# Kernel optimization log

Hardware: AMD Instinct MI355X
Metric: run time of the kernel (lower is better)

The kernel has to match this reference:

```python
import jax, jax.numpy as jnp
import numpy as np

B, P, D, H, A, C = 256, 512, 16, 256, 8, 2
HID = 256
IN_MLP = H + A + 1  # 265


def setup_inputs() -> dict:
    key = jax.random.key(0)
    ks = jax.random.split(key, 12)
    s = 0.05  # small init for recurrent stability
    return {
        "particles": jax.random.normal(ks[0], (B, P, D), jnp.float32),
        "weights": jax.random.uniform(ks[1], (B, P), jnp.float32),
        "actions": jax.random.normal(ks[2], (B, A), jnp.float32),
        "time": jax.random.uniform(ks[3], (B,), jnp.float32) * 100.0,
        "Wi": jax.random.normal(ks[4], (D + 1, 3 * H), jnp.float32) * s,
        "bi": jnp.zeros((3 * H,), jnp.float32),
        "Wh_rz": jax.random.normal(ks[5], (H, 2 * H), jnp.float32) * s,
        "Wh_n": jax.random.normal(ks[6], (H, H), jnp.float32) * s,
        "bn": jnp.zeros((H,), jnp.float32),
        "mlp_W1": jax.random.normal(ks[7], (C, IN_MLP, HID), jnp.float32) * s,
        "mlp_b1": jnp.zeros((C, HID), jnp.float32),
        "mlp_W2": jax.random.normal(ks[8], (C, HID, HID), jnp.float32) * s,
        "mlp_b2": jnp.zeros((C, HID), jnp.float32),
        "mlp_W3": jax.random.normal(ks[9], (C, HID, 1), jnp.float32) * s,
        "mlp_b3": jnp.zeros((C, 1), jnp.float32),
        "num_time_steps": 100,
    }


def reference(particles, weights, actions, time, Wi, bi, Wh_rz, Wh_n, bn,
              mlp_W1, mlp_b1, mlp_W2, mlp_b2, mlp_W3, mlp_b3, num_time_steps):
    # feature_fn = identity; append weights as an extra feature channel
    x = jnp.concatenate([particles, weights[..., None]], axis=-1)  # [B, P, D+1]
    xs = jnp.swapaxes(x, 0, 1)  # [P, B, D+1], scan over particle axis

    def gru_step(h, xt):
        gi = xt @ Wi + bi  # [B, 3H]
        i_r, i_z, i_n = jnp.split(gi, 3, axis=-1)
        hrz = h @ Wh_rz  # [B, 2H], no bias (flax GRUCell hidden r/z dense)
        r = jax.nn.sigmoid(i_r + hrz[:, :H])
        z = jax.nn.sigmoid(i_z + hrz[:, H:])
        n = jnp.tanh(i_n + r * (h @ Wh_n + bn))
        h_new = (1.0 - z) * n + z * h
        return h_new, None

    h0 = jnp.zeros((particles.shape[0], H), particles.dtype)
    enc, _ = jax.lax.scan(gru_step, h0, xs)  # last hidden == take(outputs, -1, axis=-2)

    norm_time = time / num_time_steps
    hidden = jnp.concatenate([enc, actions, norm_time[..., None]], axis=-1)  # [B, IN_MLP]

    # n_critics MLPs evaluated batched over critic axis c
    h1 = jax.nn.relu(jnp.einsum('bi,cio->bco', hidden, mlp_W1) + mlp_b1)
    h2 = jax.nn.relu(jnp.einsum('bci,cio->bco', h1, mlp_W2) + mlp_b2)
    q = jnp.einsum('bci,cio->bco', h2, mlp_W3) + mlp_b3  # [B, C, 1]
    return q[..., 0]  # [B, C]
```

## Files before the change

### kernel.cpp

```cpp
#include <hip/hip_runtime.h>
#include <hip/hip_fp16.h>

typedef _Float16 h2v __attribute__((ext_vector_type(2)));
typedef _Float16 f16x8 __attribute__((ext_vector_type(8)));
typedef float f32x4 __attribute__((ext_vector_type(4)));
typedef unsigned int u32;
typedef unsigned short u16;

#define NB 256
#define NP 512
#define NH 256

#define OFF_WH 0
#define LEN_WH 98304
#define OFF_WIB (OFF_WH + LEN_WH)
#define LEN_WIB 12288
#define OFF_W1 (OFF_WIB + LEN_WIB)
#define LEN_W1 68096
#define OFF_W2 (OFF_W1 + LEN_W1)
#define LEN_W2 65536
#define OFF_W3 (OFF_W2 + LEN_W2)
#define LEN_W3 256
#define WS_DWORDS (OFF_W3 + LEN_W3)

__device__ __forceinline__ u32 pack2(float lo, float hi) {
    h2v v; v.x = (_Float16)lo; v.y = (_Float16)hi;
    return __builtin_bit_cast(u32, v);
}

__device__ __forceinline__ float fdot2(u32 a, u32 b, float c) {
#if __has_builtin(__builtin_amdgcn_fdot2)
    return __builtin_amdgcn_fdot2(__builtin_bit_cast(h2v, a),
                                  __builtin_bit_cast(h2v, b), c, false);
#else
    h2v x = __builtin_bit_cast(h2v, a), y = __builtin_bit_cast(h2v, b);
    return c + (float)x.x * (float)y.x + (float)x.y * (float)y.y;
#endif
}

__global__ __launch_bounds__(256) void pack_kernel(
    const float* __restrict__ Wi, const float* __restrict__ Whrz,
    const float* __restrict__ Whn, const float* __restrict__ W1,
    const float* __restrict__ W2, const float* __restrict__ W3,
    u32* __restrict__ ws)
{
    for (int F = blockIdx.x * 256 + threadIdx.x; F < WS_DWORDS; F += gridDim.x * 256) {
        u32 val;
        if (F < OFF_WIB) {
            int l = F & 63; int t = F >> 6;
            int i = t % 192; int w = t / 192;
            int g = i >> 6; int tt = i & 63;
            int col = g * 256 + w * 32 + (l & 31);
            int k = ((l >> 5) << 7) + 2 * tt;
            float lo, hi;
            if (col < 512) { lo = Whrz[k * 512 + col]; hi = Whrz[(k + 1) * 512 + col]; }
            else { lo = Whn[k * 256 + (col - 512)]; hi = Whn[(k + 1) * 256 + (col - 512)]; }
            val = pack2(lo, hi);
        } else if (F < OFF_W1) {
            int j = F - OFF_WIB;
            int d = j & 3; int r = j >> 2;
            int l = r & 63; int q = r >> 6;
            int t = q % 6; int w = q / 6;
            int g = t >> 1, c = t & 1;
            int k = ((l >> 4) << 3) + 2 * d;
            int col = g * 256 + w * 32 + c * 16 + (l & 15);
            float lo = (k < 17) ? Wi[k * 768 + col] : 0.f;
            float hi = (k + 1 < 17) ? Wi[(k + 1) * 768 + col] : 0.f;
            val = pack2(lo, hi);
        } else if (F < OFF_W2) {
            int j = F - OFF_W1; int c = j / (133 * 256); int r = j % (133 * 256);
            int kk = r >> 8; int o = r & 255;
            int k = 2 * kk;
            float lo = W1[(c * 265 + k) * 256 + o];
            float hi = (k + 1 < 265) ? W1[(c * 265 + k + 1) * 256 + o] : 0.f;
            val = pack2(lo, hi);
        } else if (F < OFF_W3) {
            int j = F - OFF_W2; int c = j >> 15; int r = j & 32767;
            int kk = r >> 8; int o = r & 255;
            float lo = W2[(c * 256 + 2 * kk) * 256 + o];
            float hi = W2[(c * 256 + 2 * kk + 1) * 256 + o];
            val = pack2(lo, hi);
        } else {
            int j = F - OFF_W3; int c = j >> 7; int jj = j & 127;
            float lo = W3[c * 256 + 2 * jj];
            float hi = W3[c * 256 + 2 * jj + 1];
            val = pack2(lo, hi);
        }
        ws[F] = val;
    }
}

__global__ __launch_bounds__(512, 2) void qnet_kernel(
    const float* __restrict__ particles, const float* __restrict__ pweights,
    const float* __restrict__ actions, const float* __restrict__ timev,
    const float* __restrict__ bi, const float* __restrict__ bn,
    const float* __restrict__ b1, const float* __restrict__ b2,
    const float* __restrict__ b3, const int* __restrict__ nts,
    const u32* __restrict__ ws, float* __restrict__ out)
{
    __shared__ __align__(16) u32 sX[NP * 16];
    __shared__ __align__(16) float sG[8 * 1536];
    __shared__ __align__(16) u16 sH2[2][NH];
    __shared__ __align__(16) float sHf[NH];
    __shared__ __align__(16) float sMisc[16];

    const int b = blockIdx.x;
    const int tid = threadIdx.x;
    const int lane = tid & 63;
    const int wid = tid >> 6;

    u32 wreg[192];
    {
        const u32* gp = ws + OFF_WH + (wid * 192) * 64 + lane;
        #pragma unroll
        for (int i = 0; i < 192; ++i) wreg[i] = gp[i * 64];
    }
    {
        const float2* pr2 = (const float2*)(particles + (long)b * NP * 16);
        for (int j = tid; j < NP * 8; j += 512) {
            int p = j >> 3, q = j & 7;
            float2 v = pr2[j];
            sX[p * 16 + q] = pack2(v.x, v.y);
        }
        const float* wr = pweights + (long)b * NP;
        for (int j = tid; j < NP * 8; j += 512) {
            int p = j >> 3, q = j & 7;
            sX[p * 16 + 8 + q] = (q == 0) ? pack2(wr[p], 0.f) : 0u;
        }
    }
    if (tid < 256) ((u32*)sH2)[tid] = 0u;
    if (tid < 8) sMisc[tid] = actions[b * 8 + tid];
    if (tid == 8) sMisc[8] = timev[b] / (float)nts[0];

    float birL = 0.f, bizL = 0.f, binnL = 0.f, bnnL = 0.f, hreg = 0.f;
    if (lane < 32) {
        int j = wid * 32 + lane;
        birL = bi[j]; bizL = bi[NH + j]; binnL = bi[2 * NH + j]; bnnL = bn[j];
    }
    __syncthreads();

    const uint4* wibp = (const uint4*)(ws + OFF_WIB) + (wid * 6) * 64 + lane;

    #pragma unroll 1
    for (int p = 0; p < NP; ++p) {
        if ((p & 15) == 0) {
            f16x8 av = __builtin_bit_cast(f16x8,
                ((const uint4*)sX)[(p + (lane & 15)) * 4 + (lane >> 4)]);
            f32x4 z4 = {0.f, 0.f, 0.f, 0.f};
            int sb = (lane >> 4) << 2;
            float* gw = sG + wid * 1536 + (lane & 15);
            {
                f32x4 g0 = __builtin_amdgcn_mfma_f32_16x16x32_f16(av, __builtin_bit_cast(f16x8, wibp[0 * 64]), z4, 0, 0, 0);
                f32x4 g1 = __builtin_amdgcn_mfma_f32_16x16x32_f16(av, __builtin_bit_cast(f16x8, wibp[1 * 64]), z4, 0, 0, 0);
                #pragma unroll
                for (int r = 0; r < 4; ++r) {
                    gw[(sb + r) * 32]      = g0[r];
                    gw[(sb + r) * 32 + 16] = g1[r];
                }
            }
            {
                f32x4 g2 = __builtin_amdgcn_mfma_f32_16x16x32_f16(av, __builtin_bit_cast(f16x8, wibp[2 * 64]), z4, 0, 0, 0);
                f32x4 g3 = __builtin_amdgcn_mfma_f32_16x16x32_f16(av, __builtin_bit_cast(f16x8, wibp[3 * 64]), z4, 0, 0, 0);
                #pragma unroll
                for (int r = 0; r < 4; ++r) {
                    gw[512 + (sb + r) * 32]      = g2[r];
                    gw[512 + (sb + r) * 32 + 16] = g3[r];
                }
            }
            {
                f32x4 g4 = __builtin_amdgcn_mfma_f32_16x16x32_f16(av, __builtin_bit_cast(f16x8, wibp[4 * 64]), z4, 0, 0, 0);
                f32x4 g5 = __builtin_amdgcn_mfma_f32_16x16x32_f16(av, __builtin_bit_cast(f16x8, wibp[5 * 64]), z4, 0, 0, 0);
                #pragma unroll
                for (int r = 0; r < 4; ++r) {
                    gw[1024 + (sb + r) * 32]      = g4[r];
                    gw[1024 + (sb + r) * 32 + 16] = g5[r];
                }
            }
            __syncthreads();
        }

        float gR, gZ, gN;
        {
            const float* gp = sG + wid * 1536 + (p & 15) * 32 + (lane & 31);
            gR = gp[0]; gZ = gp[512]; gN = gp[1024];
        }

        const u32* hsrc = (const u32*)(&sH2[p & 1][0]) + ((lane >> 5) << 6);
        float aR = 0.f, aZ = 0.f, aN = 0.f;
        #pragma unroll
        for (int c = 0; c < 8; ++c) {
            uint4 h0 = ((const uint4*)hsrc)[2 * c];
            uint4 h1 = ((const uint4*)hsrc)[2 * c + 1];
            u32 hv[8] = {h0.x, h0.y, h0.z, h0.w, h1.x, h1.y, h1.z, h1.w};
            #pragma unroll
            for (int j = 0; j < 8; ++j) {
                int i = c * 8 + j;
                aR = fdot2(wreg[i],       hv[j], aR);
                aZ = fdot2(wreg[64 + i],  hv[j], aZ);
                aN = fdot2(wreg[128 + i], hv[j], aN);
            }
        }
        aR += __shfl_xor(aR, 32);
        aZ += __shfl_xor(aZ, 32);
        aN += __shfl_xor(aN, 32);

        if (lane < 32) {
            float xr = gR + birL + aR;
            float xz = gZ + bizL + aZ;
            float xn = gN + binnL;
            float r = 1.f / (1.f + __expf(-xr));
            float z = 1.f / (1.f + __expf(-xz));
            float targ = xn + r * (aN + bnnL);
            float e2 = __expf(2.f * targ);
            float n = 1.f - 2.f / (e2 + 1.f);
            hreg = (1.f - z) * n + z * hreg;
            _Float16 hh = (_Float16)hreg;
            sH2[(p + 1) & 1][wid * 32 + lane] = __builtin_bit_cast(u16, hh);
        }
        __syncthreads();
    }

    if (lane < 32) sHf[wid * 32 + lane] = hreg;
    __syncthreads();
    u32* sHid = (u32*)sG;
    u16* sL1 = (u16*)(sG + 512);
    u16* sL2 = (u16*)(sG + 1024);
    if (tid < 128) sHid[tid] = pack2(sHf[2 * tid], sHf[2 * tid + 1]);
    else if (tid < 132) { int i = tid - 128; sHid[tid] = pack2(sMisc[2 * i], sMisc[2 * i + 1]); }
    else if (tid == 132) sHid[132] = pack2(sMisc[8], 0.f);
    __syncthreads();
    {
        int c = tid >> 8, o = tid & 255;
        float acc = b1[c * 256 + o];
        const u32* wp = ws + OFF_W1 + c * 133 * 256 + o;
        #pragma unroll 4
        for (int kk = 0; kk < 133; ++kk) acc = fdot2(wp[kk * 256], sHid[kk], acc);
        acc = fmaxf(acc, 0.f);
        _Float16 a16 = (_Float16)acc;
        sL1[tid] = __builtin_bit_cast(u16, a16);
    }
    __syncthreads();
    {
        int c = tid >> 8, o = tid & 255;
        float acc = b2[c * 256 + o];
        const u32* wp = ws + OFF_W2 + c * 128 * 256 + o;
        const u32* hp = (const u32*)sL1 + c * 128;
        #pragma unroll 4
        for (int kk = 0; kk < 128; ++kk) acc = fdot2(wp[kk * 256], hp[kk], acc);
        acc = fmaxf(acc, 0.f);
        _Float16 a16 = (_Float16)acc;
        sL2[tid] = __builtin_bit_cast(u16, a16);
    }
    __syncthreads();
    if (tid < 128) {
        int c = tid >> 6, l = tid & 63;
        const u32* wp = ws + OFF_W3 + c * 128;
        const u32* hp = (const u32*)sL2 + c * 128;
        float acc = fdot2(wp[l], hp[l], 0.f);
        acc = fdot2(wp[64 + l], hp[64 + l], acc);
        #pragma unroll
        for (int off = 32; off > 0; off >>= 1) acc += __shfl_down(acc, off);
        if (l == 0) out[b * 2 + c] = acc + b3[c];
    }
}

extern "C" void kernel_launch(void* const* d_in, const int* in_sizes, int n_in,
                              void* d_out, int out_size, void* d_ws, size_t ws_size,
                              hipStream_t stream) {
    const float* particles = (const float*)d_in[0];
    const float* pweights  = (const float*)d_in[1];
    const float* actions   = (const float*)d_in[2];
    const float* timev     = (const float*)d_in[3];
    const float* Wi        = (const float*)d_in[4];
    const float* bi        = (const float*)d_in[5];
    const float* Whrz      = (const float*)d_in[6];
    const float* Whn       = (const float*)d_in[7];
    const float* bn        = (const float*)d_in[8];
    const float* W1        = (const float*)d_in[9];
    const float* b1        = (const float*)d_in[10];
    const float* W2        = (const float*)d_in[11];
    const float* b2        = (const float*)d_in[12];
    const float* W3        = (const float*)d_in[13];
    const float* b3        = (const float*)d_in[14];
    const int*   nts       = (const int*)d_in[15];
    u32* ws = (u32*)d_ws;
    float* outp = (float*)d_out;

    pack_kernel<<<(WS_DWORDS + 255) / 256, 256, 0, stream>>>(Wi, Whrz, Whn, W1, W2, W3, ws);
    qnet_kernel<<<NB, 512, 0, stream>>>(particles, pweights, actions, timev,
                                        bi, bn, b1, b2, b3, nts, ws, outp);
}
```

Baseline: 742.9 us.

## Compute GRU recurrent matvec with MFMA using AGPR-resident weight fragments

Replaces the per-lane fdot2 recurrent matvec (h @ Wh) with 16x16x32 f16 MFMA instructions issued via inline asm. Weight fragments stay in AGPRs, and the pack kernel is changed to emit the matching B-operand layout. Each wave runs 48 MFMAs per step, where only row 0 of each output tile is useful, and the cross-half shuffle reduction is removed. The goal is to shorten the serial per-step latency of the 512-step recurrence. In exchange it wastes most of the MFMA work and adds hand-placed s_nop hazard padding.

```diff
diff --git a/kernel.cpp b/kernel.cpp
--- a/kernel.cpp
+++ b/kernel.cpp
@@ -47,11 +47,13 @@
     for (int F = blockIdx.x * 256 + threadIdx.x; F < WS_DWORDS; F += gridDim.x * 256) {
         u32 val;
         if (F < OFF_WIB) {
-            int l = F & 63; int t = F >> 6;
-            int i = t % 192; int w = t / 192;
-            int g = i >> 6; int tt = i & 63;
-            int col = g * 256 + w * 32 + (l & 31);
-            int k = ((l >> 5) << 7) + 2 * tt;
+            int d = F & 3; int r = F >> 2;
+            int l = r & 63; int q = r >> 6;
+            int f = q % 48; int w = q / 48;
+            int t = f >> 3; int kt = f & 7;
+            int g = t >> 1, c = t & 1;
+            int k = kt * 32 + ((l >> 4) << 3) + 2 * d;
+            int col = g * 256 + w * 32 + c * 16 + (l & 15);
             float lo, hi;
             if (col < 512) { lo = Whrz[k * 512 + col]; hi = Whrz[(k + 1) * 512 + col]; }
             else { lo = Whn[k * 256 + (col - 512)]; hi = Whn[(k + 1) * 256 + (col - 512)]; }
@@ -89,6 +91,10 @@
         ws[F] = val;
     }
 }
+
+#define MFMA_A(acc, hv, bf) \
+    asm volatile("v_mfma_f32_16x16x32_f16 %0, %1, %2, %0" \
+                 : "+a"(acc) : "v"(hv), "a"(bf))
 
 __global__ __launch_bounds__(512, 2) void qnet_kernel(
     const float* __restrict__ particles, const float* __restrict__ pweights,
@@ -109,11 +115,11 @@
     const int lane = tid & 63;
     const int wid = tid >> 6;
 
-    u32 wreg[192];
+    f16x8 bfh[48];
     {
-        const u32* gp = ws + OFF_WH + (wid * 192) * 64 + lane;
+        const uint4* gp = (const uint4*)(ws + OFF_WH) + (wid * 48) * 64 + lane;
         #pragma unroll
-        for (int i = 0; i < 192; ++i) wreg[i] = gp[i * 64];
+        for (int i = 0; i < 48; ++i) bfh[i] = __builtin_bit_cast(f16x8, gp[i * 64]);
     }
     {
         const float2* pr2 = (const float2*)(particles + (long)b * NP * 16);
@@ -185,32 +191,48 @@
             gR = gp[0]; gZ = gp[512]; gN = gp[1024];
         }
 
-        const u32* hsrc = (const u32*)(&sH2[p & 1][0]) + ((lane >> 5) << 6);
-        float aR = 0.f, aZ = 0.f, aN = 0.f;
-        #pragma unroll
-        for (int c = 0; c < 8; ++c) {
-            uint4 h0 = ((const uint4*)hsrc)[2 * c];
-            uint4 h1 = ((const uint4*)hsrc)[2 * c + 1];
-            u32 hv[8] = {h0.x, h0.y, h0.z, h0.w, h1.x, h1.y, h1.z, h1.w};
+        const uint4* hbuf = (const uint4*)(&sH2[p & 1][0]);
+        const int hq = lane >> 4;
+
+        float s0r, s0z, s0n, s1r, s1z, s1n;
+        {
+            f32x4 a0 = {0.f, 0.f, 0.f, 0.f}, a1 = a0, a2 = a0;
+            asm volatile("s_nop 3" : "+a"(a0), "+a"(a1), "+a"(a2));
             #pragma unroll
-            for (int j = 0; j < 8; ++j) {
-                int i = c * 8 + j;
-                aR = fdot2(wreg[i],       hv[j], aR);
-                aZ = fdot2(wreg[64 + i],  hv[j], aZ);
-                aN = fdot2(wreg[128 + i], hv[j], aN);
-            }
-        }
-        aR += __shfl_xor(aR, 32);
-        aZ += __shfl_xor(aZ, 32);
-        aN += __shfl_xor(aN, 32);
-
+            for (int kt = 0; kt < 8; ++kt) {
+                f16x8 hv = __builtin_bit_cast(f16x8, hbuf[kt * 4 + hq]);
+                MFMA_A(a0, hv, bfh[kt]);
+                MFMA_A(a1, hv, bfh[16 + kt]);
+                MFMA_A(a2, hv, bfh[32 + kt]);
+            }
+            asm volatile("s_nop 7\n\ts_nop 7" : "+a"(a0), "+a"(a1), "+a"(a2));
+            s0r = a0[0]; s0z = a1[0]; s0n = a2[0];
+        }
+        {
+            f32x4 a0 = {0.f, 0.f, 0.f, 0.f}, a1 = a0, a2 = a0;
+            asm volatile("s_nop 3" : "+a"(a0), "+a"(a1), "+a"(a2));
+            #pragma unroll
+            for (int kt = 0; kt < 8; ++kt) {
+                f16x8 hv = __builtin_bit_cast(f16x8, hbuf[kt * 4 + hq]);
+                MFMA_A(a0, hv, bfh[8 + kt]);
+                MFMA_A(a1, hv, bfh[24 + kt]);
+                MFMA_A(a2, hv, bfh[40 + kt]);
+            }
+            asm volatile("s_nop 7\n\ts_nop 7" : "+a"(a0), "+a"(a1), "+a"(a2));
+            s1r = a0[0]; s1z = a1[0]; s1n = a2[0];
+        }
+
+        bool hic = (lane & 16) != 0;
+        float srm = hic ? s1r : s0r;
+        float szm = hic ? s1z : s0z;
+        float snm = hic ? s1n : s0n;
         if (lane < 32) {
-            float xr = gR + birL + aR;
-            float xz = gZ + bizL + aZ;
+            float xr = gR + birL + srm;
+            float xz = gZ + bizL + szm;
             float xn = gN + binnL;
             float r = 1.f / (1.f + __expf(-xr));
             float z = 1.f / (1.f + __expf(-xz));
-            float targ = xn + r * (aN + bnnL);
+            float targ = xn + r * (snm + bnnL);
             float e2 = __expf(2.f * targ);
             float n = 1.f - 2.f / (e2 + 1.f);
             hreg = (1.f - z) * n + z * hreg;
```

Result: slower. 921.7 us (+24.1%).

## Split GRU recurrence across 1024 threads with 16-column-per-wave ownership

Applied to the files above, without the earlier changes.

Doubles the block to 1024 threads (16 waves), so each wave owns 16 hidden columns instead of 32. Each lane now holds 96 register weights instead of 192, and the K dimension is split four ways, which needs two shuffle reductions. The hidden-state buffer gets a padded layout to avoid LDS bank conflicts on the uint4 reads. The aim is to shorten the serial per-step dot-product chain, at the cost of an extra shuffle per gate and heavier synchronization across 16 waves per step.

```diff
diff --git a/kernel.cpp b/kernel.cpp
--- a/kernel.cpp
+++ b/kernel.cpp
@@ -10,6 +10,7 @@
 #define NB 256
 #define NP 512
 #define NH 256
+#define NT 1024
 
 #define OFF_WH 0
 #define LEN_WH 98304
@@ -48,10 +49,10 @@
         u32 val;
         if (F < OFF_WIB) {
             int l = F & 63; int t = F >> 6;
-            int i = t % 192; int w = t / 192;
-            int g = i >> 6; int tt = i & 63;
-            int col = g * 256 + w * 32 + (l & 31);
-            int k = ((l >> 5) << 7) + 2 * tt;
+            int i = t % 96; int w = t / 96;
+            int g = i >> 5; int tt = i & 31;
+            int col = g * 256 + w * 16 + (l & 15);
+            int k = ((l >> 4) << 6) + 2 * tt;
             float lo, hi;
             if (col < 512) { lo = Whrz[k * 512 + col]; hi = Whrz[(k + 1) * 512 + col]; }
             else { lo = Whn[k * 256 + (col - 512)]; hi = Whn[(k + 1) * 256 + (col - 512)]; }
@@ -59,11 +60,10 @@
         } else if (F < OFF_W1) {
             int j = F - OFF_WIB;
             int d = j & 3; int r = j >> 2;
-            int l = r & 63; int q = r >> 6;
-            int t = q % 6; int w = q / 6;
-            int g = t >> 1, c = t & 1;
+            int l = r & 63; int q2 = r >> 6;
+            int g = q2 % 3; int w = q2 / 3;
             int k = ((l >> 4) << 3) + 2 * d;
-            int col = g * 256 + w * 32 + c * 16 + (l & 15);
+            int col = g * 256 + w * 16 + (l & 15);
             float lo = (k < 17) ? Wi[k * 768 + col] : 0.f;
             float hi = (k + 1 < 17) ? Wi[(k + 1) * 768 + col] : 0.f;
             val = pack2(lo, hi);
@@ -90,7 +90,7 @@
     }
 }
 
-__global__ __launch_bounds__(512, 2) void qnet_kernel(
+__global__ __launch_bounds__(1024, 4) void qnet_kernel(
     const float* __restrict__ particles, const float* __restrict__ pweights,
     const float* __restrict__ actions, const float* __restrict__ timev,
     const float* __restrict__ bi, const float* __restrict__ bn,
@@ -99,8 +99,8 @@
     const u32* __restrict__ ws, float* __restrict__ out)
 {
     __shared__ __align__(16) u32 sX[NP * 16];
-    __shared__ __align__(16) float sG[8 * 1536];
-    __shared__ __align__(16) u16 sH2[2][NH];
+    __shared__ __align__(16) float sG[16 * 768];
+    __shared__ __align__(16) u32 sH2[2][144];
     __shared__ __align__(16) float sHf[NH];
     __shared__ __align__(16) float sMisc[16];
 
@@ -109,37 +109,38 @@
     const int lane = tid & 63;
     const int wid = tid >> 6;
 
-    u32 wreg[192];
+    u32 wreg[96];
     {
-        const u32* gp = ws + OFF_WH + (wid * 192) * 64 + lane;
+        const u32* gp = ws + OFF_WH + (wid * 96) * 64 + lane;
         #pragma unroll
-        for (int i = 0; i < 192; ++i) wreg[i] = gp[i * 64];
+        for (int i = 0; i < 96; ++i) wreg[i] = gp[i * 64];
     }
     {
         const float2* pr2 = (const float2*)(particles + (long)b * NP * 16);
-        for (int j = tid; j < NP * 8; j += 512) {
+        for (int j = tid; j < NP * 8; j += NT) {
             int p = j >> 3, q = j & 7;
             float2 v = pr2[j];
             sX[p * 16 + q] = pack2(v.x, v.y);
         }
         const float* wr = pweights + (long)b * NP;
-        for (int j = tid; j < NP * 8; j += 512) {
+        for (int j = tid; j < NP * 8; j += NT) {
             int p = j >> 3, q = j & 7;
             sX[p * 16 + 8 + q] = (q == 0) ? pack2(wr[p], 0.f) : 0u;
         }
     }
-    if (tid < 256) ((u32*)sH2)[tid] = 0u;
+    if (tid < 288) ((u32*)sH2)[tid] = 0u;
     if (tid < 8) sMisc[tid] = actions[b * 8 + tid];
     if (tid == 8) sMisc[8] = timev[b] / (float)nts[0];
 
     float birL = 0.f, bizL = 0.f, binnL = 0.f, bnnL = 0.f, hreg = 0.f;
-    if (lane < 32) {
-        int j = wid * 32 + lane;
+    if (lane < 16) {
+        int j = wid * 16 + lane;
         birL = bi[j]; bizL = bi[NH + j]; binnL = bi[2 * NH + j]; bnnL = bn[j];
     }
     __syncthreads();
 
-    const uint4* wibp = (const uint4*)(ws + OFF_WIB) + (wid * 6) * 64 + lane;
+    const int hq4 = (lane >> 4) * 9;
+    const uint4* wibp = (const uint4*)(ws + OFF_WIB) + (wid * 3) * 64 + lane;
 
     #pragma unroll 1
     for (int p = 0; p < NP; ++p) {
@@ -148,63 +149,53 @@
                 ((const uint4*)sX)[(p + (lane & 15)) * 4 + (lane >> 4)]);
             f32x4 z4 = {0.f, 0.f, 0.f, 0.f};
             int sb = (lane >> 4) << 2;
-            float* gw = sG + wid * 1536 + (lane & 15);
+            float* gw = sG + wid * 768 + (lane & 15);
             {
-                f32x4 g0 = __builtin_amdgcn_mfma_f32_16x16x32_f16(av, __builtin_bit_cast(f16x8, wibp[0 * 64]), z4, 0, 0, 0);
-                f32x4 g1 = __builtin_amdgcn_mfma_f32_16x16x32_f16(av, __builtin_bit_cast(f16x8, wibp[1 * 64]), z4, 0, 0, 0);
+                f16x8 wib0 = __builtin_bit_cast(f16x8, wibp[0]);
+                f32x4 g0 = __builtin_amdgcn_mfma_f32_16x16x32_f16(av, wib0, z4, 0, 0, 0);
                 #pragma unroll
-                for (int r = 0; r < 4; ++r) {
-                    gw[(sb + r) * 32]      = g0[r];
-                    gw[(sb + r) * 32 + 16] = g1[r];
-                }
+                for (int r = 0; r < 4; ++r) gw[(sb + r) * 16] = g0[r];
             }
             {
-                f32x4 g2 = __builtin_amdgcn_mfma_f32_16x16x32_f16(av, __builtin_bit_cast(f16x8, wibp[2 * 64]), z4, 0, 0, 0);
-                f32x4 g3 = __builtin_amdgcn_mfma_f32_16x16x32_f16(av, __builtin_bit_cast(f16x8, wibp[3 * 64]), z4, 0, 0, 0);
+                f16x8 wib1 = __builtin_bit_cast(f16x8, wibp[64]);
+                f32x4 g1 = __builtin_amdgcn_mfma_f32_16x16x32_f16(av, wib1, z4, 0, 0, 0);
                 #pragma unroll
-                for (int r = 0; r < 4; ++r) {
-                    gw[512 + (sb + r) * 32]      = g2[r];
-                    gw[512 + (sb + r) * 32 + 16] = g3[r];
-                }
+                for (int r = 0; r < 4; ++r) gw[256 + (sb + r) * 16] = g1[r];
             }
             {
-                f32x4 g4 = __builtin_amdgcn_mfma_f32_16x16x32_f16(av, __builtin_bit_cast(f16x8, wibp[4 * 64]), z4, 0, 0, 0);
-                f32x4 g5 = __builtin_amdgcn_mfma_f32_16x16x32_f16(av, __builtin_bit_cast(f16x8, wibp[5 * 64]), z4, 0, 0, 0);
+                f16x8 wib2 = __builtin_bit_cast(f16x8, wibp[128]);
+                f32x4 g2 = __builtin_amdgcn_mfma_f32_16x16x32_f16(av, wib2, z4, 0, 0, 0);
                 #pragma unroll
-                for (int r = 0; r < 4; ++r) {
-                    gw[1024 + (sb + r) * 32]      = g4[r];
-                    gw[1024 + (sb + r) * 32 + 16] = g5[r];
-                }
+                for (int r = 0; r < 4; ++r) gw[512 + (sb + r) * 16] = g2[r];
             }
             __syncthreads();
         }
 
         float gR, gZ, gN;
         {
-            const float* gp = sG + wid * 1536 + (p & 15) * 32 + (lane & 31);
-            gR = gp[0]; gZ = gp[512]; gN = gp[1024];
-        }
-
-        const u32* hsrc = (const u32*)(&sH2[p & 1][0]) + ((lane >> 5) << 6);
+            const float* gp = sG + wid * 768 + (p & 15) * 16 + (lane & 15);
+            gR = gp[0]; gZ = gp[256]; gN = gp[512];
+        }
+
+        const uint4* hb = (const uint4*)(&sH2[p & 1][0]);
         float aR = 0.f, aZ = 0.f, aN = 0.f;
         #pragma unroll
         for (int c = 0; c < 8; ++c) {
-            uint4 h0 = ((const uint4*)hsrc)[2 * c];
-            uint4 h1 = ((const uint4*)hsrc)[2 * c + 1];
-            u32 hv[8] = {h0.x, h0.y, h0.z, h0.w, h1.x, h1.y, h1.z, h1.w};
+            uint4 hvv = hb[hq4 + c];
+            u32 hv[4] = {hvv.x, hvv.y, hvv.z, hvv.w};
             #pragma unroll
-            for (int j = 0; j < 8; ++j) {
-                int i = c * 8 + j;
-                aR = fdot2(wreg[i],       hv[j], aR);
-                aZ = fdot2(wreg[64 + i],  hv[j], aZ);
-                aN = fdot2(wreg[128 + i], hv[j], aN);
-            }
-        }
-        aR += __shfl_xor(aR, 32);
-        aZ += __shfl_xor(aZ, 32);
-        aN += __shfl_xor(aN, 32);
-
-        if (lane < 32) {
+            for (int j = 0; j < 4; ++j) {
+                int t = c * 4 + j;
+                aR = fdot2(wreg[t],      hv[j], aR);
+                aZ = fdot2(wreg[32 + t], hv[j], aZ);
+                aN = fdot2(wreg[64 + t], hv[j], aN);
+            }
+        }
+        aR += __shfl_xor(aR, 16); aR += __shfl_xor(aR, 32);
+        aZ += __shfl_xor(aZ, 16); aZ += __shfl_xor(aZ, 32);
+        aN += __shfl_xor(aN, 16); aN += __shfl_xor(aN, 32);
+
+        if (lane < 16) {
             float xr = gR + birL + aR;
             float xz = gZ + bizL + aZ;
             float xn = gN + binnL;
@@ -215,12 +206,13 @@
             float n = 1.f - 2.f / (e2 + 1.f);
             hreg = (1.f - z) * n + z * hreg;
             _Float16 hh = (_Float16)hreg;
-            sH2[(p + 1) & 1][wid * 32 + lane] = __builtin_bit_cast(u16, hh);
+            int di = (wid >> 2) * 36 + (wid & 3) * 8 + (lane >> 1);
+            ((u16*)&sH2[(p + 1) & 1][0])[di * 2 + (lane & 1)] = __builtin_bit_cast(u16, hh);
         }
         __syncthreads();
     }
 
-    if (lane < 32) sHf[wid * 32 + lane] = hreg;
+    if (lane < 16) sHf[wid * 16 + lane] = hreg;
     __syncthreads();
     u32* sHid = (u32*)sG;
     u16* sL1 = (u16*)(sG + 512);
@@ -229,7 +221,7 @@
     else if (tid < 132) { int i = tid - 128; sHid[tid] = pack2(sMisc[2 * i], sMisc[2 * i + 1]); }
     else if (tid == 132) sHid[132] = pack2(sMisc[8], 0.f);
     __syncthreads();
-    {
+    if (tid < 512) {
         int c = tid >> 8, o = tid & 255;
         float acc = b1[c * 256 + o];
         const u32* wp = ws + OFF_W1 + c * 133 * 256 + o;
@@ -240,7 +232,7 @@
         sL1[tid] = __builtin_bit_cast(u16, a16);
     }
     __syncthreads();
-    {
+    if (tid < 512) {
         int c = tid >> 8, o = tid & 255;
         float acc = b2[c * 256 + o];
         const u32* wp = ws + OFF_W2 + c * 128 * 256 + o;
@@ -287,6 +279,6 @@
     float* outp = (float*)d_out;
 
     pack_kernel<<<(WS_DWORDS + 255) / 256, 256, 0, stream>>>(Wi, Whrz, Whn, W1, W2, W3, ws);
-    qnet_kernel<<<NB, 512, 0, stream>>>(particles, pweights, actions, timev,
-                                        bi, bn, b1, b2, b3, nts, ws, outp);
-}
+    qnet_kernel<<<NB, NT, 0, stream>>>(particles, pweights, actions, timev,
+                                       bi, bn, b1, b2, b3, nts, ws, outp);
+}
```

Result: slower. 845.0 us (+13.7%).
